# Kernel tuning notes

Hardware: AMD Instinct MI355X
Metric: run time of the kernel (lower is better)

Reference implementation:

```python
import jax, jax.numpy as jnp
from jax import lax
import numpy as np

B, S, T = 128, 512, 64
START_TAG, STOP_TAG = T - 2, T - 1


def setup_inputs() -> dict:
    key = jax.random.key(0)
    k1, k2, k3, k4 = jax.random.split(key, 4)
    feats = jax.random.normal(k1, (B, S, T), dtype=jnp.float32)
    lengths = jax.random.randint(k2, (B,), S // 4, S + 1)
    mask = (jnp.arange(S)[None, :] < lengths[:, None])  # (B, S) bool, contiguous prefix
    tags = jax.random.randint(k3, (B, S), 0, T - 2)  # gold tags never START/STOP
    transitions = 0.1 * jax.random.normal(k4, (T, T), dtype=jnp.float32)
    transitions = transitions.at[:, START_TAG].set(-10000.0)
    transitions = transitions.at[STOP_TAG, :].set(-10000.0)
    return {"feats": feats, "mask": mask, "tags": tags, "transitions": transitions}


def reference(feats, mask, tags, transitions):
    """Viterbi decode (CRF.forward). Returns decode_idx (B, S) int32.

    scores[s,b,i,j] = feats[s,b,j] + transitions[i,j]  (i = prev tag, j = cur tag)
    """
    batch, seq_len, tag_size = feats.shape
    feats_t = jnp.transpose(feats, (1, 0, 2))      # (S, B, T)
    mask_t = jnp.transpose(mask, (1, 0))           # (S, B)
    lengths = jnp.sum(mask.astype(jnp.int32), axis=1)  # (B,)

    # t = 0: start from START_TAG row
    part0 = feats_t[0] + transitions[START_TAG][None, :]  # (B, T)

    def step(partition, inp):
        f_t, m_t = inp  # (B, T), (B,)
        # cur[b,i,j] = feats[t,b,j] + trans[i,j] + partition[b,i]
        cur = f_t[:, None, :] + transitions[None, :, :] + partition[:, :, None]
        new_part = jnp.max(cur, axis=1)                       # (B, T)
        bp = jnp.argmax(cur, axis=1).astype(jnp.int32)        # (B, T)
        bp = jnp.where(m_t[:, None], bp, 0)                   # zero bp past seq end
        return new_part, (new_part, bp)

    _, (parts, bps) = lax.scan(step, part0, (feats_t[1:], mask_t[1:]))
    partition_history = jnp.concatenate([part0[None], parts], axis=0)  # (S, B, T)

    # gather partition at the last valid position of each sequence
    last_pos = lengths - 1  # (B,)
    last_partition = jnp.take_along_axis(
        partition_history, last_pos[None, :, None], axis=0)[0]  # (B, T)

    last_values = last_partition[:, :, None] + transitions[None, :, :]  # (B, T, T)
    last_bp = jnp.argmax(last_values, axis=1).astype(jnp.int32)         # (B, T)
    pointer0 = last_bp[:, STOP_TAG]                                     # (B,)

    # back_points: bps for t=1..S-1 plus a zero pad row -> (S, B, T)
    back_points = jnp.concatenate(
        [bps, jnp.zeros((1, batch, tag_size), jnp.int32)], axis=0)
    # scatter pointer0 at time index (length-1) across the tag dim
    time_idx = jnp.arange(seq_len)[:, None]  # (S, 1)
    at_last = (time_idx == last_pos[None, :])[:, :, None]  # (S, B, 1)
    back_points = jnp.where(at_last, pointer0[None, :, None], back_points)

    # backtrack: decode[S-1]=pointer0; for idx S-2..0: pointer = bp[idx][b, pointer]
    def back_step(pointer, bp_t):
        new_ptr = jnp.take_along_axis(bp_t, pointer[:, None], axis=1)[:, 0]
        return new_ptr, new_ptr

    _, dec_rev = lax.scan(back_step, pointer0, back_points[:-1][::-1])
    decode = jnp.concatenate([dec_rev[::-1], pointer0[None]], axis=0)  # (S, B)
    return jnp.transpose(decode, (1, 0))  # (B, S)
```

## Files before the change

### kernel.cpp

```cpp
#include <hip/hip_runtime.h>

#define SEQ 512
#define TAGS 64
#define NB 128
#define START_TAG 62
#define STOP_TAG 63

__device__ __forceinline__ float readlane_f(float v, int lane) {
    return __int_as_float(__builtin_amdgcn_readlane(__float_as_int(v), lane));
}

template<int W>
__device__ __forceinline__ void partial_max(float pv, const float (&tw)[16], float fcur,
                                            float& best, int& bidx) {
#pragma unroll
    for (int k = 0; k < 16; ++k) {
        float tmp = fcur + tw[k];
        float pi  = readlane_f(pv, W * 16 + k);
        float val = tmp + pi;
        if (val > best) { best = val; bidx = W * 16 + k; }
    }
}

__global__ __launch_bounds__(256) void crf_viterbi(const float* __restrict__ feats,
                                                   const void* __restrict__ maskp,
                                                   const float* __restrict__ trans,
                                                   int* __restrict__ out) {
    __shared__ float pval[2][4][TAGS];
    __shared__ int   pidx[2][4][TAGS];
    __shared__ unsigned char bp[SEQ * TAGS];

    const int b    = blockIdx.x;
    const int tid  = threadIdx.x;
    const int lane = tid & 63;
    const int w    = tid >> 6;

    int lsum = 0;
    {
        const int* mi = (const int*)maskp;
        int w0 = mi[0];
        if (w0 == 1) {
            const int* row = mi + b * SEQ;
#pragma unroll
            for (int r = 0; r < 8; ++r) lsum += row[lane + 64 * r];
        } else if (w0 == 0x01010101) {
            const int* row = (const int*)((const unsigned char*)maskp + b * SEQ);
#pragma unroll
            for (int r = 0; r < 2; ++r) {
                int v = row[lane + 64 * r];
                lsum += (v & 1) + ((v >> 8) & 1) + ((v >> 16) & 1) + ((v >> 24) & 1);
            }
        } else {
            const float* row = (const float*)maskp + b * SEQ;
            float fa = 0.f;
#pragma unroll
            for (int r = 0; r < 8; ++r) fa += row[lane + 64 * r];
            lsum = (int)fa;
        }
#pragma unroll
        for (int off = 32; off >= 1; off >>= 1) lsum += __shfl_xor(lsum, off);
    }
    const int L = __builtin_amdgcn_readfirstlane(lsum);

    float tw[16];
#pragma unroll
    for (int k = 0; k < 16; ++k) tw[k] = trans[(w * 16 + k) * TAGS + lane];
    const float tstop  = trans[lane * TAGS + STOP_TAG];
    const float tstart = trans[START_TAG * TAGS + lane];

    const float* frow = feats + (size_t)b * SEQ * TAGS;
    float pv = frow[lane] + tstart;

    float fnext = frow[TAGS + lane];
    int buf = 0;
    for (int t = 1; t < L; ++t) {
        float fcur = fnext;
        int tn = (t + 1 < SEQ) ? (t + 1) : t;
        fnext = frow[tn * TAGS + lane];

        float best = -3.4e38f; int bidx = 0;
        switch (w) {
            case 0:  partial_max<0>(pv, tw, fcur, best, bidx); break;
            case 1:  partial_max<1>(pv, tw, fcur, best, bidx); break;
            case 2:  partial_max<2>(pv, tw, fcur, best, bidx); break;
            default: partial_max<3>(pv, tw, fcur, best, bidx); break;
        }
        pval[buf][w][lane] = best;
        pidx[buf][w][lane] = bidx;

        asm volatile("s_waitcnt lgkmcnt(0)" ::: "memory");
        __builtin_amdgcn_s_barrier();

        float b0 = pval[buf][0][lane]; int i0 = pidx[buf][0][lane];
        float b1 = pval[buf][1][lane]; int i1 = pidx[buf][1][lane];
        float b2 = pval[buf][2][lane]; int i2 = pidx[buf][2][lane];
        float b3 = pval[buf][3][lane]; int i3 = pidx[buf][3][lane];
        float bb = b0; int bi = i0;
        if (b1 > bb) { bb = b1; bi = i1; }
        if (b2 > bb) { bb = b2; bi = i2; }
        if (b3 > bb) { bb = b3; bi = i3; }
        if (w == 0) bp[t * TAGS + lane] = (unsigned char)bi;
        pv = bb;
        buf ^= 1;
    }

    float v = pv + tstop; int idx = lane;
#pragma unroll
    for (int off = 32; off >= 1; off >>= 1) {
        float ov = __shfl_xor(v, off);
        int   oi = __shfl_xor(idx, off);
        bool take = (ov > v) || (ov == v && oi < idx);
        v   = take ? ov : v;
        idx = take ? oi : idx;
    }
    const int ptr0 = __builtin_amdgcn_readfirstlane(idx);

    int* outrow = out + b * SEQ;
    for (int t = tid; t < SEQ; t += 256) {
        if (t == L - 1 || t == SEQ - 1) outrow[t] = ptr0;
        else if (t > L - 1)             outrow[t] = 0;
    }

    if (w == 0) {
        int ptr = ptr0;
        int t = L - 2;
        while (t >= 7) {
            int r0 = bp[(t + 1) * TAGS + lane];
            int r1 = bp[(t    ) * TAGS + lane];
            int r2 = bp[(t - 1) * TAGS + lane];
            int r3 = bp[(t - 2) * TAGS + lane];
            int r4 = bp[(t - 3) * TAGS + lane];
            int r5 = bp[(t - 4) * TAGS + lane];
            int r6 = bp[(t - 5) * TAGS + lane];
            int r7 = bp[(t - 6) * TAGS + lane];
            ptr = __builtin_amdgcn_readlane(r0, ptr); if (lane == 0) outrow[t    ] = ptr;
            ptr = __builtin_amdgcn_readlane(r1, ptr); if (lane == 0) outrow[t - 1] = ptr;
            ptr = __builtin_amdgcn_readlane(r2, ptr); if (lane == 0) outrow[t - 2] = ptr;
            ptr = __builtin_amdgcn_readlane(r3, ptr); if (lane == 0) outrow[t - 3] = ptr;
            ptr = __builtin_amdgcn_readlane(r4, ptr); if (lane == 0) outrow[t - 4] = ptr;
            ptr = __builtin_amdgcn_readlane(r5, ptr); if (lane == 0) outrow[t - 5] = ptr;
            ptr = __builtin_amdgcn_readlane(r6, ptr); if (lane == 0) outrow[t - 6] = ptr;
            ptr = __builtin_amdgcn_readlane(r7, ptr); if (lane == 0) outrow[t - 7] = ptr;
            t -= 8;
        }
        while (t >= 0) {
            ptr = bp[(t + 1) * TAGS + ptr];
            if (lane == 0) outrow[t] = ptr;
            t--;
        }
    }
}

extern "C" void kernel_launch(void* const* d_in, const int* in_sizes, int n_in,
                              void* d_out, int out_size, void* d_ws, size_t ws_size,
                              hipStream_t stream) {
    const float* feats = (const float*)d_in[0];
    const void*  maskp = d_in[1];
    const float* trans = (const float*)d_in[3];
    int* out = (int*)d_out;
    crf_viterbi<<<NB, 256, 0, stream>>>(feats, maskp, trans, out);
}
```

Baseline: 345.1 us.

## Tree-reduce per-wave argmax, hoist wave switch, prefetch feats in double-buffered chunks

The per-wave 16-way max/argmax becomes a pairwise tree instead of a serial compare chain, which shortens the dependency chain on each sequential Viterbi step. The switch on wave index moves outside the time loop, so each wave runs a specialized loop. Feature rows are loaded in two register banks of four steps, giving loads more lead time before they are used. The tree reduction can change tie-breaking when values are equal, and the chunked loop raises register pressure and code size.

Result: slower. 957.5 us (+177.5%).

```diff
diff --git a/kernel.cpp b/kernel.cpp
--- a/kernel.cpp
+++ b/kernel.cpp
@@ -5,21 +5,97 @@
 #define NB 128
 #define START_TAG 62
 #define STOP_TAG 63
+#define CHUNK 4
 
 __device__ __forceinline__ float readlane_f(float v, int lane) {
     return __int_as_float(__builtin_amdgcn_readlane(__float_as_int(v), lane));
 }
 
 template<int W>
-__device__ __forceinline__ void partial_max(float pv, const float (&tw)[16], float fcur,
-                                            float& best, int& bidx) {
+__device__ __forceinline__ void step_partial(float pv, const float (&tw)[16], float fcur,
+                                             float& best, int& bidx) {
+    float v[16]; int id[16];
 #pragma unroll
     for (int k = 0; k < 16; ++k) {
-        float tmp = fcur + tw[k];
-        float pi  = readlane_f(pv, W * 16 + k);
-        float val = tmp + pi;
-        if (val > best) { best = val; bidx = W * 16 + k; }
-    }
+        float a = fcur + tw[k];
+        v[k]  = a + readlane_f(pv, W * 16 + k);
+        id[k] = W * 16 + k;
+    }
+#pragma unroll
+    for (int s = 1; s < 16; s <<= 1) {
+#pragma unroll
+        for (int k0 = 0; k0 < 16; k0 += 2 * s) {
+            bool c = v[k0 + s] > v[k0];
+            v[k0]  = c ? v[k0 + s]  : v[k0];
+            id[k0] = c ? id[k0 + s] : id[k0];
+        }
+    }
+    best = v[0]; bidx = id[0];
+}
+
+template<int W>
+__device__ __forceinline__ void do_step(int t, int lane, float& pv, int& buf,
+                                        const float (&tw)[16], float fcur,
+                                        float (*pval)[4][TAGS], int (*pidx)[4][TAGS],
+                                        unsigned char* bp) {
+    float best; int bidx;
+    step_partial<W>(pv, tw, fcur, best, bidx);
+    pval[buf][W][lane] = best;
+    pidx[buf][W][lane] = bidx;
+    asm volatile("s_waitcnt lgkmcnt(0)" ::: "memory");
+    __builtin_amdgcn_s_barrier();
+    float b0 = pval[buf][0][lane]; int i0 = pidx[buf][0][lane];
+    float b1 = pval[buf][1][lane]; int i1 = pidx[buf][1][lane];
+    float b2 = pval[buf][2][lane]; int i2 = pidx[buf][2][lane];
+    float b3 = pval[buf][3][lane]; int i3 = pidx[buf][3][lane];
+    float bb = b0; int bi = i0;
+    if (b1 > bb) { bb = b1; bi = i1; }
+    if (b2 > bb) { bb = b2; bi = i2; }
+    if (b3 > bb) { bb = b3; bi = i3; }
+    if (W == 0) bp[t * TAGS + lane] = (unsigned char)bi;
+    pv = bb;
+    buf ^= 1;
+}
+
+template<int W>
+__device__ __forceinline__ float forward_loop(const float* __restrict__ frow, int L, int lane,
+                                              const float (&tw)[16], float pv,
+                                              float (*pval)[4][TAGS], int (*pidx)[4][TAGS],
+                                              unsigned char* bp) {
+    float fA[CHUNK], fB[CHUNK];
+#pragma unroll
+    for (int r = 0; r < CHUNK; ++r) fA[r] = frow[(1 + r) * TAGS + lane];
+#pragma unroll
+    for (int r = 0; r < CHUNK; ++r) fB[r] = frow[(1 + CHUNK + r) * TAGS + lane];
+    int buf = 0;
+    int t0 = 1;
+    for (;;) {
+#pragma unroll
+        for (int r = 0; r < CHUNK; ++r) {
+            int t = t0 + r;
+            if (t < L) do_step<W>(t, lane, pv, buf, tw, fA[r], pval, pidx, bp);
+        }
+#pragma unroll
+        for (int r = 0; r < CHUNK; ++r) {
+            int tr = t0 + 2 * CHUNK + r; tr = tr < SEQ ? tr : SEQ - 1;
+            fA[r] = frow[tr * TAGS + lane];
+        }
+        t0 += CHUNK;
+        if (t0 >= L) break;
+#pragma unroll
+        for (int r = 0; r < CHUNK; ++r) {
+            int t = t0 + r;
+            if (t < L) do_step<W>(t, lane, pv, buf, tw, fB[r], pval, pidx, bp);
+        }
+#pragma unroll
+        for (int r = 0; r < CHUNK; ++r) {
+            int tr = t0 + 2 * CHUNK + r; tr = tr < SEQ ? tr : SEQ - 1;
+            fB[r] = frow[tr * TAGS + lane];
+        }
+        t0 += CHUNK;
+        if (t0 >= L) break;
+    }
+    return pv;
 }
 
 __global__ __launch_bounds__(256) void crf_viterbi(const float* __restrict__ feats,
@@ -71,37 +147,11 @@
     const float* frow = feats + (size_t)b * SEQ * TAGS;
     float pv = frow[lane] + tstart;
 
-    float fnext = frow[TAGS + lane];
-    int buf = 0;
-    for (int t = 1; t < L; ++t) {
-        float fcur = fnext;
-        int tn = (t + 1 < SEQ) ? (t + 1) : t;
-        fnext = frow[tn * TAGS + lane];
-
-        float best = -3.4e38f; int bidx = 0;
-        switch (w) {
-            case 0:  partial_max<0>(pv, tw, fcur, best, bidx); break;
-            case 1:  partial_max<1>(pv, tw, fcur, best, bidx); break;
-            case 2:  partial_max<2>(pv, tw, fcur, best, bidx); break;
-            default: partial_max<3>(pv, tw, fcur, best, bidx); break;
-        }
-        pval[buf][w][lane] = best;
-        pidx[buf][w][lane] = bidx;
-
-        asm volatile("s_waitcnt lgkmcnt(0)" ::: "memory");
-        __builtin_amdgcn_s_barrier();
-
-        float b0 = pval[buf][0][lane]; int i0 = pidx[buf][0][lane];
-        float b1 = pval[buf][1][lane]; int i1 = pidx[buf][1][lane];
-        float b2 = pval[buf][2][lane]; int i2 = pidx[buf][2][lane];
-        float b3 = pval[buf][3][lane]; int i3 = pidx[buf][3][lane];
-        float bb = b0; int bi = i0;
-        if (b1 > bb) { bb = b1; bi = i1; }
-        if (b2 > bb) { bb = b2; bi = i2; }
-        if (b3 > bb) { bb = b3; bi = i3; }
-        if (w == 0) bp[t * TAGS + lane] = (unsigned char)bi;
-        pv = bb;
-        buf ^= 1;
+    switch (w) {
+        case 0:  pv = forward_loop<0>(frow, L, lane, tw, pv, pval, pidx, bp); break;
+        case 1:  pv = forward_loop<1>(frow, L, lane, tw, pv, pval, pidx, bp); break;
+        case 2:  pv = forward_loop<2>(frow, L, lane, tw, pv, pval, pidx, bp); break;
+        default: pv = forward_loop<3>(frow, L, lane, tw, pv, pval, pidx, bp); break;
     }
 
     float v = pv + tstop; int idx = lane;
```
